# Kernel tuning notes

Hardware: AMD Instinct MI355X
Metric: run time of the kernel (lower is better)

Reference implementation:

```python
import jax, jax.numpy as jnp
import numpy as np

N_SITES = 128
BOND = 64
PHYS = 2
BATCH = 8192
EPS = 1e-30


def setup_inputs() -> dict:
    key = jax.random.key(0)
    k0, k1, k2, k3 = jax.random.split(key, 4)
    std = 1.0 / np.sqrt(BOND)  # default init_std in _normal_init
    return {
        "configurations": jax.random.randint(k0, (BATCH, N_SITES), 0, PHYS),
        "left_tensor": jax.random.normal(k1, (1, PHYS, BOND), jnp.float32) * std,
        "bulk_tensors": jax.random.normal(k2, (N_SITES - 2, BOND, PHYS, BOND), jnp.float32) * std,
        "right_tensor": jax.random.normal(k3, (BOND, PHYS, 1), jnp.float32) * std,
    }


def _log_amplitude_squared(left, bulk, right, configs):
    # left: (1,P,D), bulk: (N-2,D,P,D), right: (D,P,1), configs: (B,N) int
    env = left[0, configs[:, 0], :]                         # (B, D)
    m = jnp.clip(jnp.max(jnp.abs(env), axis=1), EPS, None)  # (B,)
    env = env / m[:, None]
    log_scale = jnp.log(m)

    def step(carry, xs):
        env, ls = carry
        A, v = xs                                # A: (D,P,D), v: (B,)
        sel = A[:, v, :]                         # (D, B, D) gathered matrices
        env = jnp.einsum('bi,ibj->bj', env, sel)  # (B, D) batched matvec
        m = jnp.clip(jnp.max(jnp.abs(env), axis=1), EPS, None)
        env = env / m[:, None]
        return (env, ls + jnp.log(m)), None

    (env, log_scale), _ = jax.lax.scan(
        step, (env, log_scale), (bulk, configs[:, 1:-1].T))

    sel = right[:, configs[:, -1], 0]            # (D, B)
    psi = jnp.einsum('bd,db->b', env, sel)       # (B,) rescaled amplitude
    m = jnp.clip(jnp.abs(psi), EPS, None)
    psi = psi / m
    log_scale = log_scale + jnp.log(m)

    abs2 = jnp.clip(psi * psi, EPS, None)
    return jnp.log(abs2) + 2.0 * log_scale      # (B,) log|Psi(v)|^2


def reference(configurations, left_tensor, bulk_tensors, right_tensor):
    return _log_amplitude_squared(left_tensor, bulk_tensors, right_tensor, configurations)
```

## Files before the change

### kernel.cpp

```cpp
#include <hip/hip_runtime.h>
#include <math.h>
#include <stdint.h>

typedef __attribute__((ext_vector_type(8))) short bf16x8;
typedef __attribute__((ext_vector_type(4))) float f32x4;
typedef __attribute__((ext_vector_type(4))) int   i32x4;
typedef __attribute__((ext_vector_type(2))) int   i32x2;

#define NSITES 128
#define NBULK  126
#define BOND   64
#define BATCH  8192

#define WSITE     49152
#define WMASK_OFF ((size_t)NBULK * (size_t)WSITE)
#define WS_NEED   (WMASK_OFF + (size_t)BATCH * 16)

#define EBUF_SZ 12288
#define RED_OFF 24576
#define SMEM_SZ 25088

#define MFMA_BF16 __builtin_amdgcn_mfma_f32_16x16x32_bf16

__global__ void prep_w(const float* __restrict__ bulk, char* __restrict__ wsd) {
    const int s  = blockIdx.x;
    const int t  = threadIdx.x;
    const int jt = (t >> 6) & 3;
    const int l  = t & 63;
    const int j  = jt * 16 + (l & 15);
    const int kb0 = (l >> 4) * 8;
    const float* bs = bulk + (size_t)s * 8192;
    char* dsite = wsd + (size_t)s * WSITE;
    #pragma unroll
    for (int ks = 0; ks < 2; ++ks) {
        const int kb = ks * 32 + kb0;
        #pragma unroll
        for (int v = 0; v < 2; ++v) {
            uint h[3][8];
            #pragma unroll
            for (int e = 0; e < 8; ++e) {
                const float x = bs[(size_t)(kb + e) * 128 + v * 64 + j];
                const uint  u1 = __float_as_uint(x) & 0xffff0000u;
                const float r1 = x - __uint_as_float(u1);
                const uint  u2 = __float_as_uint(r1) & 0xffff0000u;
                const float r2 = r1 - __uint_as_float(u2);
                h[0][e] = u1; h[1][e] = u2;
                h[2][e] = __float_as_uint(r2) & 0xffff0000u;
            }
            #pragma unroll
            for (int tm = 0; tm < 3; ++tm) {
                i32x4 q;
                q.x = (int)((h[tm][0] >> 16) | (h[tm][1] & 0xffff0000u));
                q.y = (int)((h[tm][2] >> 16) | (h[tm][3] & 0xffff0000u));
                q.z = (int)((h[tm][4] >> 16) | (h[tm][5] & 0xffff0000u));
                q.w = (int)((h[tm][6] >> 16) | (h[tm][7] & 0xffff0000u));
                *(i32x4*)(dsite + ((((v*3+tm)*2+ks)*4 + jt) * 1024) + l * 16) = q;
            }
        }
    }
}

__global__ void prep_mask(const int* __restrict__ cfg, uint* __restrict__ msk) {
    const int w = threadIdx.x >> 6, l = threadIdx.x & 63;
    const int b = blockIdx.x * 2 + (w >> 1);
    const int half = w & 1;
    int idx = half * 64 + l + 1;
    if (idx > 127) idx = 127;
    const int v = cfg[b * NSITES + idx];
    const unsigned long long bal = __ballot(v != 0);
    if (l == 0) {
        msk[b * 4 + half * 2]     = (uint)(bal & 0xffffffffu);
        msk[b * 4 + half * 2 + 1] = (uint)(bal >> 32);
    }
}


#define LOADA_(P,V,T,K) \
    asm volatile("global_load_dwordx4 %0, %1, off" \
                 : "=v"(A_##P##_##V##T##K) \
                 : "v"(gp_ + aG[V][T][K]) : "memory")
#define LOADA(P,V,T,K) LOADA_(P,V,T,K)

#define PREFETCH_ASM(S, NP) do { \
    const char* gp_ = ws + (size_t)(((S) < NBULK) ? (S) : 0) * WSITE; \
    LOADA(NP,0,0,0); LOADA(NP,0,0,1); LOADA(NP,0,1,0); LOADA(NP,0,1,1); \
    LOADA(NP,0,2,0); LOADA(NP,0,2,1); LOADA(NP,1,0,0); LOADA(NP,1,0,1); \
    LOADA(NP,1,1,0); LOADA(NP,1,1,1); LOADA(NP,1,2,0); LOADA(NP,1,2,1); \
} while (0)

#define AF_(P,V,T,K) (__builtin_bit_cast(bf16x8, A_##P##_##V##T##K))
#define AF(P,V,T,K) AF_(P,V,T,K)

#define PUBLISH(PW) do { \
    uint pa_[3][4]; \
    _Pragma("unroll") \
    for (int r = 0; r < 4; ++r) { \
        const float x_ = eg0[r]; \
        const uint  u1_ = __float_as_uint(x_) & 0xffff0000u; \
        const float r1_ = x_ - __uint_as_float(u1_); \
        const uint  u2_ = __float_as_uint(r1_) & 0xffff0000u; \
        const float r2_ = r1_ - __uint_as_float(u2_); \
        pa_[0][r] = u1_; pa_[1][r] = u2_; \
        pa_[2][r] = __float_as_uint(r2_) & 0xffff0000u; \
    } \
    _Pragma("unroll") \
    for (int tm = 0; tm < 3; ++tm) { \
        i32x2 d_; \
        d_.x = (int)((pa_[tm][0] >> 16) | (pa_[tm][1] & 0xffff0000u)); \
        d_.y = (int)((pa_[tm][2] >> 16) | (pa_[tm][3] & 0xffff0000u)); \
        *(i32x2*)(smem + aW[PW] + tm * 2048) = d_; \
    } \
    _Pragma("unroll") \
    for (int r = 0; r < 4; ++r) { \
        const float x_ = eg1[r]; \
        const uint  u1_ = __float_as_uint(x_) & 0xffff0000u; \
        const float r1_ = x_ - __uint_as_float(u1_); \
        const uint  u2_ = __float_as_uint(r1_) & 0xffff0000u; \
        const float r2_ = r1_ - __uint_as_float(u2_); \
        pa_[0][r] = u1_; pa_[1][r] = u2_; \
        pa_[2][r] = __float_as_uint(r2_) & 0xffff0000u; \
    } \
    _Pragma("unroll") \
    for (int tm = 0; tm < 3; ++tm) { \
        i32x2 d_; \
        d_.x = (int)((pa_[tm][0] >> 16) | (pa_[tm][1] & 0xffff0000u)); \
        d_.y = (int)((pa_[tm][2] >> 16) | (pa_[tm][3] & 0xffff0000u)); \
        *(i32x2*)(smem + aW[PW] + 6144 + tm * 2048) = d_; \
    } \
} while (0)

#define MSTEP(TW, TE, CUR) \
    acc00 = MFMA_BF16(AF(CUR,0,TW,0), Bf[0][TE][0], acc00, 0, 0, 0); \
    acc01 = MFMA_BF16(AF(CUR,1,TW,0), Bf[0][TE][0], acc01, 0, 0, 0); \
    acc10 = MFMA_BF16(AF(CUR,0,TW,0), Bf[1][TE][0], acc10, 0, 0, 0); \
    acc11 = MFMA_BF16(AF(CUR,1,TW,0), Bf[1][TE][0], acc11, 0, 0, 0); \
    acc00 = MFMA_BF16(AF(CUR,0,TW,1), Bf[0][TE][1], acc00, 0, 0, 0); \
    acc01 = MFMA_BF16(AF(CUR,1,TW,1), Bf[0][TE][1], acc01, 0, 0, 0); \
    acc10 = MFMA_BF16(AF(CUR,0,TW,1), Bf[1][TE][1], acc10, 0, 0, 0); \
    acc11 = MFMA_BF16(AF(CUR,1,TW,1), Bf[1][TE][1], acc11, 0, 0, 0);

#define SITE_BODY(S, II, CUR, NXT, DO_SCALE, DO_MAX) do { \
    asm volatile("s_waitcnt vmcnt(0)" ::: "memory"); \
    __builtin_amdgcn_sched_barrier(0); \
    bf16x8 Bf[2][3][2]; \
    _Pragma("unroll") for (int gg = 0; gg < 2; ++gg) \
    _Pragma("unroll") for (int tm = 0; tm < 3; ++tm) \
    _Pragma("unroll") for (int ks = 0; ks < 2; ++ks) \
        Bf[gg][tm][ks] = *(const bf16x8*)(smem + aB[CUR][ks] + (gg * 3 + tm) * 2048); \
    PREFETCH_ASM((S) + 1, NXT); \
    f32x4 acc00 = {0.f,0.f,0.f,0.f}, acc01 = {0.f,0.f,0.f,0.f}; \
    f32x4 acc10 = {0.f,0.f,0.f,0.f}, acc11 = {0.f,0.f,0.f,0.f}; \
    MSTEP(2,0,CUR) MSTEP(1,1,CUR) MSTEP(0,2,CUR) \
    MSTEP(1,0,CUR) MSTEP(0,1,CUR) MSTEP(0,0,CUR) \
    const bool v0_ = ((mwa >> (II)) & 1u) != 0u; \
    const bool v1_ = ((mwb >> (II)) & 1u) != 0u; \
    eg0.x = v0_ ? acc01.x : acc00.x;  eg0.y = v0_ ? acc01.y : acc00.y; \
    eg0.z = v0_ ? acc01.z : acc00.z;  eg0.w = v0_ ? acc01.w : acc00.w; \
    eg1.x = v1_ ? acc11.x : acc10.x;  eg1.y = v1_ ? acc11.y : acc10.y; \
    eg1.z = v1_ ? acc11.z : acc10.z;  eg1.w = v1_ ? acc11.w : acc10.w; \
    if (DO_SCALE) { \
        f32x4 m4a = *(const f32x4*)(smem + RED_OFF + lb * 16); \
        f32x4 m4b = *(const f32x4*)(smem + RED_OFF + 256 + lb * 16); \
        const float ma = fmaxf(fmaxf(m4a.x, m4a.y), fmaxf(m4a.z, m4a.w)); \
        const float mb = fmaxf(fmaxf(m4b.x, m4b.y), fmaxf(m4b.z, m4b.w)); \
        const int ea = (__float_as_int(ma) >> 23) & 255; \
        const int eb = (__float_as_int(mb) >> 23) & 255; \
        const float sa = __int_as_float((254 - ea) << 23); \
        const float sb = __int_as_float((254 - eb) << 23); \
        ls0 += (float)(ea - 127) * 0.6931471805599453f; \
        ls1 += (float)(eb - 127) * 0.6931471805599453f; \
        eg0.x *= sa; eg0.y *= sa; eg0.z *= sa; eg0.w *= sa; \
        eg1.x *= sb; eg1.y *= sb; eg1.z *= sb; eg1.w *= sb; \
    } \
    if (DO_MAX) { \
        float ma = fmaxf(fmaxf(fabsf(eg0.x), fabsf(eg0.y)), fmaxf(fabsf(eg0.z), fabsf(eg0.w))); \
        float mb = fmaxf(fmaxf(fabsf(eg1.x), fabsf(eg1.y)), fmaxf(fabsf(eg1.z), fabsf(eg1.w))); \
        ma = fmaxf(ma, __shfl_xor(ma, 16)); ma = fmaxf(ma, __shfl_xor(ma, 32)); \
        mb = fmaxf(mb, __shfl_xor(mb, 16)); mb = fmaxf(mb, __shfl_xor(mb, 32)); \
        if (lg == 0) { \
            *(float*)(smem + RED_OFF + lb * 16 + jt * 4) = ma; \
            *(float*)(smem + RED_OFF + 256 + lb * 16 + jt * 4) = mb; \
        } \
    } \
    PUBLISH(NXT); \
    __syncthreads(); \
} while (0)

#define RUN_CHUNK(CB, MWE0, MWE1, CNT, SC0, MXE) { \
    const uint mwa = (MWE0), mwb = (MWE1); \
    _Pragma("unroll 1") \
    for (int i2 = 0; i2 < (CNT); i2 += 2) { \
        SITE_BODY((CB) * 32 + i2,     i2,     0, 1, ((SC0) && i2 == 0),           false); \
        SITE_BODY((CB) * 32 + i2 + 1, i2 + 1, 1, 0, false, ((MXE) && i2 == (CNT) - 2)); \
    } \
}

__global__ __launch_bounds__(256, 1) void mps_main(
    const int*   __restrict__ cfg,
    const float* __restrict__ left,
    const float* __restrict__ right,
    const char*  __restrict__ ws,
    float*       __restrict__ out)
{
    extern __shared__ __align__(16) char smem[];
    const int t  = threadIdx.x;
    const int w  = t >> 6, l = t & 63;
    const int lg = l >> 4, lb = l & 15;
    const int jt = w;
    const int bbase = blockIdx.x * 32;
    const int b0 = bbase + lb, b1 = bbase + 16 + lb;

    int aG[2][3][2];
    #pragma unroll
    for (int vv = 0; vv < 2; ++vv)
        #pragma unroll
        for (int tm = 0; tm < 3; ++tm)
            #pragma unroll
            for (int ks = 0; ks < 2; ++ks)
                aG[vv][tm][ks] = (((vv*3+tm)*2 + ks)*4 + jt) * 1024 + l * 16;

    int aB[2][2], aW[2];
    {
        const int key = lb & 7;
        const int s0 = ((0 + lg) ^ key) * 16;
        const int s1 = ((4 + lg) ^ key) * 16;
        aB[0][0] = lb * 128 + s0;          aB[0][1] = lb * 128 + s1;
        aB[1][0] = aB[0][0] + EBUF_SZ;     aB[1][1] = aB[0][1] + EBUF_SZ;
        aW[0] = lb * 128 + (((jt * 2 + (lg >> 1)) ^ key) * 16) + (lg & 1) * 8;
        aW[1] = aW[0] + EBUF_SZ;
    }

    i32x4 A_0_000, A_0_001, A_0_010, A_0_011, A_0_020, A_0_021;
    i32x4 A_0_100, A_0_101, A_0_110, A_0_111, A_0_120, A_0_121;
    i32x4 A_1_000, A_1_001, A_1_010, A_1_011, A_1_020, A_1_021;
    i32x4 A_1_100, A_1_101, A_1_110, A_1_111, A_1_120, A_1_121;

    float ls0 = 0.f, ls1 = 0.f;
    f32x4 eg0 = {0.f,0.f,0.f,0.f}, eg1 = {0.f,0.f,0.f,0.f};

    PREFETCH_ASM(0, 0);

    const uint* mp = (const uint*)(ws + WMASK_OFF);
    uint4 vmg0 = *(const uint4*)(mp + (size_t)b0 * 4);
    uint4 vmg1 = *(const uint4*)(mp + (size_t)b1 * 4);
    const int c00 = cfg[b0 * NSITES], c01 = cfg[b1 * NSITES];
    const int jout = jt * 16 + lg * 4;
    #pragma unroll
    for (int r = 0; r < 4; ++r) {
        eg0[r] = left[c00 * BOND + jout + r];
        eg1[r] = left[c01 * BOND + jout + r];
    }
    PUBLISH(0);
    __syncthreads();

    RUN_CHUNK(0, vmg0.x, vmg1.x, 32, false, true)
    RUN_CHUNK(1, vmg0.y, vmg1.y, 32, true,  true)
    RUN_CHUNK(2, vmg0.z, vmg1.z, 32, true,  true)
    RUN_CHUNK(3, vmg0.w, vmg1.w, 30, true,  false)

    {
        const int vl0 = cfg[b0 * NSITES + 127], vl1 = cfg[b1 * NSITES + 127];
        float p0 = eg0.x * right[(jout + 0) * 2 + vl0] + eg0.y * right[(jout + 1) * 2 + vl0]
                 + eg0.z * right[(jout + 2) * 2 + vl0] + eg0.w * right[(jout + 3) * 2 + vl0];
        float p1 = eg1.x * right[(jout + 0) * 2 + vl1] + eg1.y * right[(jout + 1) * 2 + vl1]
                 + eg1.z * right[(jout + 2) * 2 + vl1] + eg1.w * right[(jout + 3) * 2 + vl1];
        p0 += __shfl_xor(p0, 16); p0 += __shfl_xor(p0, 32);
        p1 += __shfl_xor(p1, 16); p1 += __shfl_xor(p1, 32);
        if (lg == 0) {
            *(float*)(smem + RED_OFF + lb * 16 + jt * 4) = p0;
            *(float*)(smem + RED_OFF + 256 + lb * 16 + jt * 4) = p1;
        }
    }
    __syncthreads();
    if (w == 0 && l < 16) {
        f32x4 q0 = *(const f32x4*)(smem + RED_OFF + lb * 16);
        f32x4 q1 = *(const f32x4*)(smem + RED_OFF + 256 + lb * 16);
        const float s0 = (q0.x + q0.y) + (q0.z + q0.w);
        const float s1 = (q1.x + q1.y) + (q1.z + q1.w);
        out[b0] = 2.0f * (ls0 + logf(fmaxf(fabsf(s0), 1e-30f)));
        out[b1] = 2.0f * (ls1 + logf(fmaxf(fabsf(s1), 1e-30f)));
    }
}

#define WPB     16
#define TPB     (WPB * 64)
#define SITE_ELTS (BOND * 2 * BOND)

__global__ __launch_bounds__(TPB, 2) void mps_logamp_fp32(
    const int*   __restrict__ cfg, const float* __restrict__ left,
    const float* __restrict__ bulk, const float* __restrict__ right,
    float* __restrict__ out)
{
    __shared__ float Abuf[2][SITE_ELTS];
    __shared__ float envs[WPB][BOND];
    __shared__ int   cfgs[WPB * NSITES];
    const int t = threadIdx.x;
    const int w = t >> 6, l = t & 63;
    const int bbase = blockIdx.x * WPB;
    const int b = bbase + w;
    cfgs[t] = cfg[bbase * NSITES + t];
    cfgs[t + TPB] = cfg[bbase * NSITES + t + TPB];
    { const float4* src = (const float4*)bulk; float4* dst = (float4*)(&Abuf[0][0]);
      dst[t] = src[t]; dst[t + TPB] = src[t + TPB]; }
    __syncthreads();
    const int c0 = cfgs[w * NSITES];
    float e = left[c0 * BOND + l];
    float m = fabsf(e);
    #pragma unroll
    for (int k = 32; k; k >>= 1) m = fmaxf(m, __shfl_xor(m, k));
    m = fmaxf(m, 1e-30f);
    e = e / m;
    float ls = logf(m);
    envs[w][l] = e;
    for (int s = 0; s < NBULK; ++s) {
        const int cur = s & 1, nxt = cur ^ 1;
        const bool pf = (s + 1 < NBULK);
        float4 p0, p1;
        if (pf) { const float4* src = (const float4*)(bulk + (size_t)(s + 1) * SITE_ELTS);
                  p0 = src[t]; p1 = src[t + TPB]; }
        const int v = cfgs[w * NSITES + (s + 1)];
        const float* Ap = &Abuf[cur][v * BOND + l];
        const float* ev = &envs[w][0];
        float acc = 0.0f;
        #pragma unroll
        for (int i = 0; i < BOND; i += 4) {
            const float4 e4 = *(const float4*)(ev + i);
            acc = fmaf(e4.x, Ap[(i + 0) * 128], acc);
            acc = fmaf(e4.y, Ap[(i + 1) * 128], acc);
            acc = fmaf(e4.z, Ap[(i + 2) * 128], acc);
            acc = fmaf(e4.w, Ap[(i + 3) * 128], acc);
        }
        float mm = fabsf(acc);
        #pragma unroll
        for (int k = 32; k; k >>= 1) mm = fmaxf(mm, __shfl_xor(mm, k));
        mm = fmaxf(mm, 1e-30f);
        acc = acc / mm;
        ls += logf(mm);
        if (pf) { float4* dst = (float4*)(&Abuf[nxt][0]); dst[t] = p0; dst[t + TPB] = p1; }
        envs[w][l] = acc;
        e = acc;
        __syncthreads();
    }
    const int vl = cfgs[w * NSITES + (NSITES - 1)];
    float p = e * right[l * 2 + vl];
    #pragma unroll
    for (int k = 32; k; k >>= 1) p += __shfl_xor(p, k);
    const float am = fmaxf(fabsf(p), 1e-30f);
    if (l == 0) out[b] = 2.0f * (ls + logf(am));
}

extern "C" void kernel_launch(void* const* d_in, const int* in_sizes, int n_in,
                              void* d_out, int out_size, void* d_ws, size_t ws_size,
                              hipStream_t stream) {
    const int*   cfg   = (const int*)d_in[0];
    const float* left  = (const float*)d_in[1];
    const float* bulk  = (const float*)d_in[2];
    const float* right = (const float*)d_in[3];
    float*       out   = (float*)d_out;

    if (ws_size >= WS_NEED) {
        hipLaunchKernelGGL(prep_w, dim3(NBULK), dim3(256), 0, stream,
                           bulk, (char*)d_ws);
        hipLaunchKernelGGL(prep_mask, dim3(BATCH / 2), dim3(256), 0, stream,
                           cfg, (uint*)((char*)d_ws + WMASK_OFF));
        hipLaunchKernelGGL(mps_main, dim3(BATCH / 32), dim3(256), SMEM_SZ, stream,
                           cfg, left, right, (const char*)d_ws, out);
    } else {
        hipLaunchKernelGGL(mps_logamp_fp32, dim3(BATCH / WPB), dim3(TPB), 0, stream,
                           cfg, left, bulk, right, out);
    }
}
```

Baseline: 126.5 us.

## Software-pipeline the two batch groups so one's epilogue overlaps the other's MFMAs

The per-site loop is split into two half-phases. Each processes one 16-sample group's MFMAs while the other group's select, rescale, bf16 split and LDS publish runs, with the second group lagging by one phase. The LDS environment buffer changes from double-buffered pairs to two single per-group regions, and the four accumulator chains are split to shorten MFMA dependency chains. The prefetch wait moves to vmcnt(12), and barriers become raw s_barrier plus lgkmcnt waits. This adds twice as many barriers per site and more complex mask-shift bookkeeping, which risks extra sync overhead and ordering bugs.

```diff
diff --git a/kernel.cpp b/kernel.cpp
--- a/kernel.cpp
+++ b/kernel.cpp
@@ -16,9 +16,8 @@
 #define WMASK_OFF ((size_t)NBULK * (size_t)WSITE)
 #define WS_NEED   (WMASK_OFF + (size_t)BATCH * 16)
 
-#define EBUF_SZ 12288
-#define RED_OFF 24576
-#define SMEM_SZ 25088
+#define RED_OFF 12288
+#define SMEM_SZ 12800
 
 #define MFMA_BF16 __builtin_amdgcn_mfma_f32_16x16x32_bf16
 
@@ -81,118 +80,110 @@
                  : "v"(gp_ + aG[V][T][K]) : "memory")
 #define LOADA(P,V,T,K) LOADA_(P,V,T,K)
 
-#define PREFETCH_ASM(S, NP) do { \
+#define PREFETCH(S, P) do { \
     const char* gp_ = ws + (size_t)(((S) < NBULK) ? (S) : 0) * WSITE; \
-    LOADA(NP,0,0,0); LOADA(NP,0,0,1); LOADA(NP,0,1,0); LOADA(NP,0,1,1); \
-    LOADA(NP,0,2,0); LOADA(NP,0,2,1); LOADA(NP,1,0,0); LOADA(NP,1,0,1); \
-    LOADA(NP,1,1,0); LOADA(NP,1,1,1); LOADA(NP,1,2,0); LOADA(NP,1,2,1); \
+    LOADA(P,0,0,0); LOADA(P,0,0,1); LOADA(P,0,1,0); LOADA(P,0,1,1); \
+    LOADA(P,0,2,0); LOADA(P,0,2,1); LOADA(P,1,0,0); LOADA(P,1,0,1); \
+    LOADA(P,1,1,0); LOADA(P,1,1,1); LOADA(P,1,2,0); LOADA(P,1,2,1); \
 } while (0)
 
 #define AF_(P,V,T,K) (__builtin_bit_cast(bf16x8, A_##P##_##V##T##K))
 #define AF(P,V,T,K) AF_(P,V,T,K)
 
-#define PUBLISH(PW) do { \
-    uint pa_[3][4]; \
+#define EPI(EG, A0, A1, BIT, DOSC, DOMX, ROFF, LS, WB) do { \
+    const bool vv_ = (BIT) != 0u; \
+    EG.x = vv_ ? A1.x : A0.x; EG.y = vv_ ? A1.y : A0.y; \
+    EG.z = vv_ ? A1.z : A0.z; EG.w = vv_ ? A1.w : A0.w; \
+    if (DOSC) { \
+        f32x4 m4_ = *(const f32x4*)(smem + (ROFF) + lb * 16); \
+        const float mm_ = fmaxf(fmaxf(m4_.x, m4_.y), fmaxf(m4_.z, m4_.w)); \
+        const int ee_ = (__float_as_int(mm_) >> 23) & 255; \
+        const float sc_ = __int_as_float((254 - ee_) << 23); \
+        LS += (float)(ee_ - 127) * 0.6931471805599453f; \
+        EG.x *= sc_; EG.y *= sc_; EG.z *= sc_; EG.w *= sc_; \
+    } \
+    if (DOMX) { \
+        float mm_ = fmaxf(fmaxf(fabsf(EG.x), fabsf(EG.y)), fmaxf(fabsf(EG.z), fabsf(EG.w))); \
+        mm_ = fmaxf(mm_, __shfl_xor(mm_, 16)); mm_ = fmaxf(mm_, __shfl_xor(mm_, 32)); \
+        if (lg == 0) *(float*)(smem + (ROFF) + lb * 16 + jt * 4) = mm_; \
+    } \
+    uint p1_[4], p2_[4], p3_[4]; \
+    const float ev_[4] = {EG.x, EG.y, EG.z, EG.w}; \
     _Pragma("unroll") \
     for (int r = 0; r < 4; ++r) { \
-        const float x_ = eg0[r]; \
+        const float x_ = ev_[r]; \
         const uint  u1_ = __float_as_uint(x_) & 0xffff0000u; \
         const float r1_ = x_ - __uint_as_float(u1_); \
         const uint  u2_ = __float_as_uint(r1_) & 0xffff0000u; \
         const float r2_ = r1_ - __uint_as_float(u2_); \
-        pa_[0][r] = u1_; pa_[1][r] = u2_; \
-        pa_[2][r] = __float_as_uint(r2_) & 0xffff0000u; \
-    } \
+        p1_[r] = u1_; p2_[r] = u2_; \
+        p3_[r] = __float_as_uint(r2_) & 0xffff0000u; \
+    } \
+    { i32x2 d_; d_.x = (int)((p1_[0] >> 16) | (p1_[1] & 0xffff0000u)); \
+      d_.y = (int)((p1_[2] >> 16) | (p1_[3] & 0xffff0000u)); \
+      *(i32x2*)(smem + (WB) + aWr) = d_; } \
+    { i32x2 d_; d_.x = (int)((p2_[0] >> 16) | (p2_[1] & 0xffff0000u)); \
+      d_.y = (int)((p2_[2] >> 16) | (p2_[3] & 0xffff0000u)); \
+      *(i32x2*)(smem + (WB) + aWr + 2048) = d_; } \
+    { i32x2 d_; d_.x = (int)((p3_[0] >> 16) | (p3_[1] & 0xffff0000u)); \
+      d_.y = (int)((p3_[2] >> 16) | (p3_[3] & 0xffff0000u)); \
+      *(i32x2*)(smem + (WB) + aWr + 4096) = d_; } \
+} while (0)
+
+#define MS4(P, TW, TE, BF) \
+    q00_ = MFMA_BF16(AF(P,0,TW,0), BF[TE][0], q00_, 0, 0, 0); \
+    q10_ = MFMA_BF16(AF(P,1,TW,0), BF[TE][0], q10_, 0, 0, 0); \
+    q01_ = MFMA_BF16(AF(P,0,TW,1), BF[TE][1], q01_, 0, 0, 0); \
+    q11_ = MFMA_BF16(AF(P,1,TW,1), BF[TE][1], q11_, 0, 0, 0);
+
+#define MFMA24(A0, A1, P, BF) do { \
+    f32x4 q00_ = {0.f,0.f,0.f,0.f}, q01_ = {0.f,0.f,0.f,0.f}; \
+    f32x4 q10_ = {0.f,0.f,0.f,0.f}, q11_ = {0.f,0.f,0.f,0.f}; \
+    MS4(P,2,0,BF) MS4(P,1,1,BF) MS4(P,0,2,BF) \
+    MS4(P,1,0,BF) MS4(P,0,1,BF) MS4(P,0,0,BF) \
+    A0 = q00_ + q01_;  A1 = q10_ + q11_; \
+} while (0)
+
+#define PHASE_A(S, P, NP, BIT1, SC1, MX1) do { \
+    bf16x8 Bf_[3][2]; \
     _Pragma("unroll") \
     for (int tm = 0; tm < 3; ++tm) { \
-        i32x2 d_; \
-        d_.x = (int)((pa_[tm][0] >> 16) | (pa_[tm][1] & 0xffff0000u)); \
-        d_.y = (int)((pa_[tm][2] >> 16) | (pa_[tm][3] & 0xffff0000u)); \
-        *(i32x2*)(smem + aW[PW] + tm * 2048) = d_; \
-    } \
-    _Pragma("unroll") \
-    for (int r = 0; r < 4; ++r) { \
-        const float x_ = eg1[r]; \
-        const uint  u1_ = __float_as_uint(x_) & 0xffff0000u; \
-        const float r1_ = x_ - __uint_as_float(u1_); \
-        const uint  u2_ = __float_as_uint(r1_) & 0xffff0000u; \
-        const float r2_ = r1_ - __uint_as_float(u2_); \
-        pa_[0][r] = u1_; pa_[1][r] = u2_; \
-        pa_[2][r] = __float_as_uint(r2_) & 0xffff0000u; \
-    } \
+        Bf_[tm][0] = *(const bf16x8*)(smem + aB0 + tm * 2048); \
+        Bf_[tm][1] = *(const bf16x8*)(smem + aB1 + tm * 2048); \
+    } \
+    PREFETCH((S) + 1, NP); \
+    asm volatile("s_waitcnt vmcnt(12)" ::: "memory"); \
+    __builtin_amdgcn_sched_barrier(0); \
+    EPI(eg1, acC1_0, acC1_1, BIT1, SC1, MX1, RED_OFF + 256, ls1, 6144); \
+    MFMA24(acC0_0, acC0_1, P, Bf_); \
+    asm volatile("s_waitcnt lgkmcnt(0)" ::: "memory"); \
+    __builtin_amdgcn_s_barrier(); \
+} while (0)
+
+#define PHASE_B(S, P, BIT0, SC0, MX0) do { \
+    bf16x8 Bf_[3][2]; \
     _Pragma("unroll") \
     for (int tm = 0; tm < 3; ++tm) { \
-        i32x2 d_; \
-        d_.x = (int)((pa_[tm][0] >> 16) | (pa_[tm][1] & 0xffff0000u)); \
-        d_.y = (int)((pa_[tm][2] >> 16) | (pa_[tm][3] & 0xffff0000u)); \
-        *(i32x2*)(smem + aW[PW] + 6144 + tm * 2048) = d_; \
-    } \
-} while (0)
-
-#define MSTEP(TW, TE, CUR) \
-    acc00 = MFMA_BF16(AF(CUR,0,TW,0), Bf[0][TE][0], acc00, 0, 0, 0); \
-    acc01 = MFMA_BF16(AF(CUR,1,TW,0), Bf[0][TE][0], acc01, 0, 0, 0); \
-    acc10 = MFMA_BF16(AF(CUR,0,TW,0), Bf[1][TE][0], acc10, 0, 0, 0); \
-    acc11 = MFMA_BF16(AF(CUR,1,TW,0), Bf[1][TE][0], acc11, 0, 0, 0); \
-    acc00 = MFMA_BF16(AF(CUR,0,TW,1), Bf[0][TE][1], acc00, 0, 0, 0); \
-    acc01 = MFMA_BF16(AF(CUR,1,TW,1), Bf[0][TE][1], acc01, 0, 0, 0); \
-    acc10 = MFMA_BF16(AF(CUR,0,TW,1), Bf[1][TE][1], acc10, 0, 0, 0); \
-    acc11 = MFMA_BF16(AF(CUR,1,TW,1), Bf[1][TE][1], acc11, 0, 0, 0);
-
-#define SITE_BODY(S, II, CUR, NXT, DO_SCALE, DO_MAX) do { \
-    asm volatile("s_waitcnt vmcnt(0)" ::: "memory"); \
-    __builtin_amdgcn_sched_barrier(0); \
-    bf16x8 Bf[2][3][2]; \
-    _Pragma("unroll") for (int gg = 0; gg < 2; ++gg) \
-    _Pragma("unroll") for (int tm = 0; tm < 3; ++tm) \
-    _Pragma("unroll") for (int ks = 0; ks < 2; ++ks) \
-        Bf[gg][tm][ks] = *(const bf16x8*)(smem + aB[CUR][ks] + (gg * 3 + tm) * 2048); \
-    PREFETCH_ASM((S) + 1, NXT); \
-    f32x4 acc00 = {0.f,0.f,0.f,0.f}, acc01 = {0.f,0.f,0.f,0.f}; \
-    f32x4 acc10 = {0.f,0.f,0.f,0.f}, acc11 = {0.f,0.f,0.f,0.f}; \
-    MSTEP(2,0,CUR) MSTEP(1,1,CUR) MSTEP(0,2,CUR) \
-    MSTEP(1,0,CUR) MSTEP(0,1,CUR) MSTEP(0,0,CUR) \
-    const bool v0_ = ((mwa >> (II)) & 1u) != 0u; \
-    const bool v1_ = ((mwb >> (II)) & 1u) != 0u; \
-    eg0.x = v0_ ? acc01.x : acc00.x;  eg0.y = v0_ ? acc01.y : acc00.y; \
-    eg0.z = v0_ ? acc01.z : acc00.z;  eg0.w = v0_ ? acc01.w : acc00.w; \
-    eg1.x = v1_ ? acc11.x : acc10.x;  eg1.y = v1_ ? acc11.y : acc10.y; \
-    eg1.z = v1_ ? acc11.z : acc10.z;  eg1.w = v1_ ? acc11.w : acc10.w; \
-    if (DO_SCALE) { \
-        f32x4 m4a = *(const f32x4*)(smem + RED_OFF + lb * 16); \
-        f32x4 m4b = *(const f32x4*)(smem + RED_OFF + 256 + lb * 16); \
-        const float ma = fmaxf(fmaxf(m4a.x, m4a.y), fmaxf(m4a.z, m4a.w)); \
-        const float mb = fmaxf(fmaxf(m4b.x, m4b.y), fmaxf(m4b.z, m4b.w)); \
-        const int ea = (__float_as_int(ma) >> 23) & 255; \
-        const int eb = (__float_as_int(mb) >> 23) & 255; \
-        const float sa = __int_as_float((254 - ea) << 23); \
-        const float sb = __int_as_float((254 - eb) << 23); \
-        ls0 += (float)(ea - 127) * 0.6931471805599453f; \
-        ls1 += (float)(eb - 127) * 0.6931471805599453f; \
-        eg0.x *= sa; eg0.y *= sa; eg0.z *= sa; eg0.w *= sa; \
-        eg1.x *= sb; eg1.y *= sb; eg1.z *= sb; eg1.w *= sb; \
-    } \
-    if (DO_MAX) { \
-        float ma = fmaxf(fmaxf(fabsf(eg0.x), fabsf(eg0.y)), fmaxf(fabsf(eg0.z), fabsf(eg0.w))); \
-        float mb = fmaxf(fmaxf(fabsf(eg1.x), fabsf(eg1.y)), fmaxf(fabsf(eg1.z), fabsf(eg1.w))); \
-        ma = fmaxf(ma, __shfl_xor(ma, 16)); ma = fmaxf(ma, __shfl_xor(ma, 32)); \
-        mb = fmaxf(mb, __shfl_xor(mb, 16)); mb = fmaxf(mb, __shfl_xor(mb, 32)); \
-        if (lg == 0) { \
-            *(float*)(smem + RED_OFF + lb * 16 + jt * 4) = ma; \
-            *(float*)(smem + RED_OFF + 256 + lb * 16 + jt * 4) = mb; \
-        } \
-    } \
-    PUBLISH(NXT); \
-    __syncthreads(); \
-} while (0)
-
-#define RUN_CHUNK(CB, MWE0, MWE1, CNT, SC0, MXE) { \
-    const uint mwa = (MWE0), mwb = (MWE1); \
+        Bf_[tm][0] = *(const bf16x8*)(smem + 6144 + aB0 + tm * 2048); \
+        Bf_[tm][1] = *(const bf16x8*)(smem + 6144 + aB1 + tm * 2048); \
+    } \
+    EPI(eg0, acC0_0, acC0_1, BIT0, SC0, MX0, RED_OFF, ls0, 0); \
+    MFMA24(acC1_0, acC1_1, P, Bf_); \
+    asm volatile("s_waitcnt lgkmcnt(0)" ::: "memory"); \
+    __builtin_amdgcn_s_barrier(); \
+} while (0)
+
+#define SITEPAIR(S, I2, M0, M1S, CSC, CMX) do { \
+    PHASE_A((S),     0, 1, ((M1S) >> (I2)) & 1u,        false,               false); \
+    PHASE_B((S),     0,    ((M0)  >> (I2)) & 1u,        (CSC) && (I2) == 0,  (CMX) && (I2) == 30); \
+    PHASE_A((S) + 1, 1, 0, ((M1S) >> ((I2)+1)) & 1u,    (CSC) && (I2) == 0,  (CMX) && (I2) == 30); \
+    PHASE_B((S) + 1, 1,    ((M0)  >> ((I2)+1)) & 1u,    false,               false); \
+} while (0)
+
+#define RUN_CHUNK(CB, M0, M1S, CNT, CSC, CMX) { \
     _Pragma("unroll 1") \
-    for (int i2 = 0; i2 < (CNT); i2 += 2) { \
-        SITE_BODY((CB) * 32 + i2,     i2,     0, 1, ((SC0) && i2 == 0),           false); \
-        SITE_BODY((CB) * 32 + i2 + 1, i2 + 1, 1, 0, false, ((MXE) && i2 == (CNT) - 2)); \
-    } \
+    for (int i2 = 0; i2 < (CNT); i2 += 2) \
+        SITEPAIR((CB) * 32 + i2, i2, M0, M1S, CSC, CMX); \
 }
 
 __global__ __launch_bounds__(256, 1) void mps_main(
@@ -219,16 +210,10 @@
             for (int ks = 0; ks < 2; ++ks)
                 aG[vv][tm][ks] = (((vv*3+tm)*2 + ks)*4 + jt) * 1024 + l * 16;
 
-    int aB[2][2], aW[2];
-    {
-        const int key = lb & 7;
-        const int s0 = ((0 + lg) ^ key) * 16;
-        const int s1 = ((4 + lg) ^ key) * 16;
-        aB[0][0] = lb * 128 + s0;          aB[0][1] = lb * 128 + s1;
-        aB[1][0] = aB[0][0] + EBUF_SZ;     aB[1][1] = aB[0][1] + EBUF_SZ;
-        aW[0] = lb * 128 + (((jt * 2 + (lg >> 1)) ^ key) * 16) + (lg & 1) * 8;
-        aW[1] = aW[0] + EBUF_SZ;
-    }
+    const int key = lb & 7;
+    const int aB0 = lb * 128 + ((lg ^ key) * 16);
+    const int aB1 = lb * 128 + (((4 + lg) ^ key) * 16);
+    const int aWr = lb * 128 + (((jt * 2 + (lg >> 1)) ^ key) * 16) + (lg & 1) * 8;
 
     i32x4 A_0_000, A_0_001, A_0_010, A_0_011, A_0_020, A_0_021;
     i32x4 A_0_100, A_0_101, A_0_110, A_0_111, A_0_120, A_0_121;
@@ -236,27 +221,43 @@
     i32x4 A_1_100, A_1_101, A_1_110, A_1_111, A_1_120, A_1_121;
 
     float ls0 = 0.f, ls1 = 0.f;
-    f32x4 eg0 = {0.f,0.f,0.f,0.f}, eg1 = {0.f,0.f,0.f,0.f};
-
-    PREFETCH_ASM(0, 0);
+    f32x4 eg0, eg1, acC0_0, acC0_1, acC1_0, acC1_1;
+
+    PREFETCH(0, 0);
 
     const uint* mp = (const uint*)(ws + WMASK_OFF);
-    uint4 vmg0 = *(const uint4*)(mp + (size_t)b0 * 4);
-    uint4 vmg1 = *(const uint4*)(mp + (size_t)b1 * 4);
+    const uint4 vmg0 = *(const uint4*)(mp + (size_t)b0 * 4);
+    const uint4 vmg1 = *(const uint4*)(mp + (size_t)b1 * 4);
+    const uint s1a = vmg1.x << 1;
+    const uint s1b = (vmg1.y << 1) | (vmg1.x >> 31);
+    const uint s1c = (vmg1.z << 1) | (vmg1.y >> 31);
+    const uint s1d = (vmg1.w << 1) | (vmg1.z >> 31);
+
     const int c00 = cfg[b0 * NSITES], c01 = cfg[b1 * NSITES];
     const int jout = jt * 16 + lg * 4;
+    f32x4 ig0, ig1;
     #pragma unroll
     for (int r = 0; r < 4; ++r) {
-        eg0[r] = left[c00 * BOND + jout + r];
-        eg1[r] = left[c01 * BOND + jout + r];
-    }
-    PUBLISH(0);
-    __syncthreads();
-
-    RUN_CHUNK(0, vmg0.x, vmg1.x, 32, false, true)
-    RUN_CHUNK(1, vmg0.y, vmg1.y, 32, true,  true)
-    RUN_CHUNK(2, vmg0.z, vmg1.z, 32, true,  true)
-    RUN_CHUNK(3, vmg0.w, vmg1.w, 30, true,  false)
+        ig0[r] = left[c00 * BOND + jout + r];
+        ig1[r] = left[c01 * BOND + jout + r];
+    }
+    acC0_0 = ig0; acC0_1 = ig0;
+    acC1_0 = ig1; acC1_1 = ig1;
+    eg0 = ig0; eg1 = ig1;
+    EPI(eg0, acC0_0, acC0_1, 0u, false, false, RED_OFF, ls0, 0);
+    asm volatile("s_waitcnt lgkmcnt(0)" ::: "memory");
+    __builtin_amdgcn_s_barrier();
+
+    RUN_CHUNK(0, vmg0.x, s1a, 32, false, true)
+    RUN_CHUNK(1, vmg0.y, s1b, 32, true,  true)
+    RUN_CHUNK(2, vmg0.z, s1c, 32, true,  true)
+    RUN_CHUNK(3, vmg0.w, s1d, 30, true,  false)
+
+    {
+        const bool v_ = ((vmg1.w >> 29) & 1u) != 0u;
+        eg1.x = v_ ? acC1_1.x : acC1_0.x;  eg1.y = v_ ? acC1_1.y : acC1_0.y;
+        eg1.z = v_ ? acC1_1.z : acC1_0.z;  eg1.w = v_ ? acC1_1.w : acC1_0.w;
+    }
 
     {
         const int vl0 = cfg[b0 * NSITES + 127], vl1 = cfg[b1 * NSITES + 127];
```

New measurement: 139.5 us. 1.1x slower.
